# Kernel optimization log

Measured on AMD Instinct MI355X. Metric: run time of the kernel, lower is better.

The kernel has to match this reference:

```python
import jax, jax.numpy as jnp
import numpy as np

HIDDEN = 512
HEADS = 8
HEAD_SIZE = HIDDEN // HEADS
INF = 10000.0


def _heads(x):
    # [N, L, D] -> [N, L, H, Dh]
    return x.reshape(x.shape[0], x.shape[1], HEADS, HEAD_SIZE)


def _alpha_from_logits(logits, mask_row, mask_col):
    # logits: [N, L1, L2, H]; mask_row: [N, L1]; mask_col: [N, L2]
    pair = (mask_row[:, :, None, None] * mask_col[:, None, :, None]) > 0  # [N,L1,L2,1]
    logits = jnp.where(pair, logits, logits - INF)
    alpha = jax.nn.softmax(logits, axis=2)
    row = (mask_row[:, :, None, None]) > 0  # [N,L1,1,1]
    return jnp.where(row, alpha, jnp.zeros_like(alpha))


def setup_inputs() -> dict:
    key = jax.random.key(0)
    ks = jax.random.split(key, 10)
    N, L1, L2, D = 4, 1024, 1024, HIDDEN
    input1 = jax.random.normal(ks[0], (N, L1, D), dtype=jnp.float32)
    input2 = jax.random.normal(ks[1], (N, L2, D), dtype=jnp.float32)
    # masks: 1 for valid tokens, with some padding at the tail
    mask1 = (jnp.arange(L1)[None, :] < jnp.array([L1, L1 - 64, L1 - 128, L1 - 200])[:, None]).astype(jnp.float32)
    mask2 = (jnp.arange(L2)[None, :] < jnp.array([L2 - 32, L2, L2 - 96, L2 - 10])[:, None]).astype(jnp.float32)
    s = 1.0 / np.sqrt(D)
    Wq1 = jax.random.normal(ks[2], (D, D), dtype=jnp.float32) * s
    Wk1 = jax.random.normal(ks[3], (D, D), dtype=jnp.float32) * s
    Wv1 = jax.random.normal(ks[4], (D, D), dtype=jnp.float32) * s
    Wq2 = jax.random.normal(ks[5], (D, D), dtype=jnp.float32) * s
    Wk2 = jax.random.normal(ks[6], (D, D), dtype=jnp.float32) * s
    Wv2 = jax.random.normal(ks[7], (D, D), dtype=jnp.float32) * s
    return {"input1": input1, "mask1": mask1, "input2": input2, "mask2": mask2,
            "Wq1": Wq1, "Wk1": Wk1, "Wv1": Wv1, "Wq2": Wq2, "Wk2": Wk2, "Wv2": Wv2}


def reference(input1, mask1, input2, mask2, Wq1, Wk1, Wv1, Wq2, Wk2, Wv2):
    # nn.Linear(bias=False): x @ W.T
    q1 = _heads(input1 @ Wq1.T)
    k1 = _heads(input1 @ Wk1.T)
    v1 = _heads(input1 @ Wv1.T)
    q2 = _heads(input2 @ Wq2.T)
    k2 = _heads(input2 @ Wk2.T)
    v2 = _heads(input2 @ Wv2.T)
    logits11 = jnp.einsum('blhd,bkhd->blkh', q1, k1)
    logits12 = jnp.einsum('blhd,bkhd->blkh', q1, k2)
    logits21 = jnp.einsum('blhd,bkhd->blkh', q2, k1)
    logits22 = jnp.einsum('blhd,bkhd->blkh', q2, k2)
    a11 = _alpha_from_logits(logits11, mask1, mask1)
    a12 = _alpha_from_logits(logits12, mask1, mask2)
    a21 = _alpha_from_logits(logits21, mask2, mask1)
    a22 = _alpha_from_logits(logits22, mask2, mask2)
    N, L1 = input1.shape[0], input1.shape[1]
    L2 = input2.shape[1]
    o11 = jnp.einsum('blkh,bkhd->blhd', a11, v1).reshape(N, L1, HIDDEN)
    o12 = jnp.einsum('blkh,bkhd->blhd', a12, v2).reshape(N, L1, HIDDEN)
    o21 = jnp.einsum('blkh,bkhd->blhd', a21, v1).reshape(N, L2, HIDDEN)
    o22 = jnp.einsum('blkh,bkhd->blhd', a22, v2).reshape(N, L2, HIDDEN)
    output1 = (o11 + o12) / 2
    output2 = (o21 + o22) / 2
    return (output1, output2)
```

## Files before the change

kernel.cpp:

```cpp
#include <hip/hip_runtime.h>

#define DEV static __device__ __forceinline__

typedef unsigned short u16;
typedef short bf16x8 __attribute__((ext_vector_type(8)));
typedef u16 u16x8v __attribute__((ext_vector_type(8)));
typedef u16 u16x4v __attribute__((ext_vector_type(4)));
typedef float f32x4 __attribute__((ext_vector_type(4)));

static constexpr int NB = 4, L = 1024, D = 512, H = 8, DH = 64;
static constexpr size_t E  = (size_t)NB * L * D;
static constexpr size_t WE = (size_t)D * D;

static constexpr size_t OFF_X1H = 0;
static constexpr size_t OFF_X1L = OFF_X1H + E;
static constexpr size_t OFF_X2H = OFF_X1L + E;
static constexpr size_t OFF_X2L = OFF_X2H + E;
static constexpr size_t OFF_WH  = OFF_X2L + E;
static constexpr size_t OFF_WL  = OFF_WH + 6 * WE;
static constexpr size_t OFF_QKV = OFF_WL + 6 * WE;
static constexpr size_t OFF_VLEN = OFF_QKV + 10 * E;

DEV u16 f2bf(float x) {
    unsigned u = __builtin_bit_cast(unsigned, x);
    unsigned r = u + 0x7FFFu + ((u >> 16) & 1u);
    return (u16)(r >> 16);
}
DEV float bf2f(u16 h) {
    unsigned u = ((unsigned)h) << 16;
    return __builtin_bit_cast(float, u);
}
DEV unsigned cvtpk(float lo, float hi) {
    unsigned r;
    asm("v_cvt_pk_bf16_f32 %0, %1, %2" : "=v"(r) : "v"(lo), "v"(hi));
    return r;
}
DEV bf16x8 ldfrag(const u16* p) {
    u16x8v t = *reinterpret_cast<const u16x8v*>(p);
    return __builtin_bit_cast(bf16x8, t);
}
typedef __attribute__((address_space(1))) const unsigned gas_u32;
typedef __attribute__((address_space(3))) unsigned las_u32;
DEV void gld16(const u16* g, u16* l) {
    __builtin_amdgcn_global_load_lds((gas_u32*)g, (las_u32*)l, 16, 0, 0);
}

__global__ __launch_bounds__(256) void k_split_all(const float* __restrict__ x1,
                                                   const float* __restrict__ x2,
                                                   const float* w0, const float* w1,
                                                   const float* w2, const float* w3,
                                                   const float* w4, const float* w5,
                                                   u16* __restrict__ ws) {
    int b = blockIdx.x;
    const float* src;
    u16 *hi, *lo;
    int i0;
    if (b < 2048)      { src = x1; hi = ws + OFF_X1H; lo = ws + OFF_X1L; i0 = b; }
    else if (b < 4096) { src = x2; hi = ws + OFF_X2H; lo = ws + OFF_X2L; i0 = b - 2048; }
    else {
        int wi = (b - 4096) >> 8;
        const float* wp[6] = {w0, w1, w2, w3, w4, w5};
        src = wp[wi];
        hi = ws + OFF_WH + (size_t)wi * WE;
        lo = ws + OFF_WL + (size_t)wi * WE;
        i0 = (b - 4096) & 255;
    }
    int i = i0 * 256 + threadIdx.x;
    float4 v = reinterpret_cast<const float4*>(src)[i];
    float xs[4] = {v.x, v.y, v.z, v.w};
    u16x4v h, l;
#pragma unroll
    for (int j = 0; j < 4; j++) {
        u16 hh = f2bf(xs[j]);
        h[j] = hh;
        l[j] = f2bf(xs[j] - bf2f(hh));
    }
    int idx = i * 4;
    int m = idx >> 9, e = idx & 511;
    int o = (m << 9) | (e ^ ((m & 7) << 3));
    *reinterpret_cast<u16x4v*>(hi + o) = h;
    *reinterpret_cast<u16x4v*>(lo + o) = l;
}

__global__ __launch_bounds__(256) void k_vlen(const float* __restrict__ m1,
                                              const float* __restrict__ m2,
                                              int* __restrict__ vl) {
    int b = blockIdx.x;
    int s = b >> 2, n = b & 3;
    const float* m = (s ? m2 : m1) + n * L;
    float p = 0.f;
    for (int i = threadIdx.x; i < L; i += 256) p += m[i];
#pragma unroll
    for (int mk = 1; mk < 64; mk <<= 1) p += __shfl_xor(p, mk, 64);
    __shared__ float w4[4];
    if ((threadIdx.x & 63) == 0) w4[threadIdx.x >> 6] = p;
    __syncthreads();
    if (threadIdx.x == 0) vl[b] = (int)(w4[0] + w4[1] + w4[2] + w4[3] + 0.5f);
}

__global__ __launch_bounds__(256) void k_proj(u16* __restrict__ ws) {
    __shared__ __align__(16) u16 ta[2][128][64];
    __shared__ __align__(16) u16 tb[2][128][64];

    const int b     = blockIdx.x;
    const int proj  = b >> 7;
    const int rem   = b & 127;
    const int mtile = rem >> 2;
    const int ntile = rem & 3;
    const int tid   = threadIdx.x;
    const int w     = tid >> 6;
    const int lane  = tid & 63;
    const int lr    = lane & 15;
    const int g     = lane >> 4;
    const int wr    = w >> 1, wc = w & 1;

    const int src  = proj / 3;
    const int kind = proj % 3;
    const u16* Xh = ws + (src ? OFF_X2H : OFF_X1H);
    const u16* Xl = ws + (src ? OFF_X2L : OFF_X1L);
    const u16* Wh = ws + OFF_WH + (size_t)proj * WE;
    const u16* Wl = ws + OFF_WL + (size_t)proj * WE;

    const int m0 = mtile * 128, n0 = ntile * 128;

    const int lrow = lane >> 3, lcol = lane & 7;
    const u16* gA0 = Xh + (size_t)(m0 + w * 32 + lrow) * 512 + lcol * 8;
    const u16* gA1 = Xl + (size_t)(m0 + w * 32 + lrow) * 512 + lcol * 8;
    const u16* gB0 = Wh + (size_t)(n0 + w * 32 + lrow) * 512 + lcol * 8;
    const u16* gB1 = Wl + (size_t)(n0 + w * 32 + lrow) * 512 + lcol * 8;

    f32x4 acc[4][4];
#pragma unroll
    for (int fr = 0; fr < 4; fr++)
#pragma unroll
        for (int cb = 0; cb < 4; cb++) acc[fr][cb] = {0.f, 0.f, 0.f, 0.f};

#pragma unroll 1
    for (int step = 0; step < 8; step++) {
        __syncthreads();
#pragma unroll
        for (int i = 0; i < 4; i++) {
            const int roff = w * 32 + i * 8;
            const int e0 = step * 64;
            gld16(gA0 + e0 + i * (8 * 512), &ta[0][roff][0]);
            gld16(gA1 + e0 + i * (8 * 512), &ta[1][roff][0]);
            gld16(gB0 + e0 + i * (8 * 512), &tb[0][roff][0]);
            gld16(gB1 + e0 + i * (8 * 512), &tb[1][roff][0]);
        }
        __syncthreads();

#pragma unroll
        for (int ks = 0; ks < 2; ks++) {
            bf16x8 ah[4], al[4];
#pragma unroll
            for (int fr = 0; fr < 4; fr++) {
                const int row = wr * 64 + fr * 16 + lr;
                const int ch = (ks * 4 + g) ^ (row & 7);
                ah[fr] = ldfrag(&ta[0][row][ch * 8]);
                al[fr] = ldfrag(&ta[1][row][ch * 8]);
            }
#pragma unroll
            for (int cb = 0; cb < 4; cb++) {
                const int rowb = wc * 64 + cb * 16 + lr;
                const int chb = (ks * 4 + g) ^ (rowb & 7);
                bf16x8 bh = ldfrag(&tb[0][rowb][chb * 8]);
                bf16x8 bl = ldfrag(&tb[1][rowb][chb * 8]);
#pragma unroll
                for (int fr = 0; fr < 4; fr++) {
                    acc[fr][cb] = __builtin_amdgcn_mfma_f32_16x16x32_bf16(ah[fr], bh, acc[fr][cb], 0, 0, 0);
                    acc[fr][cb] = __builtin_amdgcn_mfma_f32_16x16x32_bf16(ah[fr], bl, acc[fr][cb], 0, 0, 0);
                    acc[fr][cb] = __builtin_amdgcn_mfma_f32_16x16x32_bf16(al[fr], bh, acc[fr][cb], 0, 0, 0);
                }
            }
        }
    }

    if (kind < 2) {
        const float qscale = (kind == 0) ? 1.4426950408889634f : 1.0f;
        u16* dhi = ws + OFF_QKV + (size_t)(src * 4 + kind * 2) * E;
        u16* dlo = dhi + E;
#pragma unroll
        for (int fr = 0; fr < 4; fr++)
#pragma unroll
            for (int cb = 0; cb < 4; cb++) {
                int d  = n0 + wc * 64 + cb * 16 + lr;
                int hh = d >> 6, dh = d & 63;
#pragma unroll
                for (int r = 0; r < 4; r++) {
                    int m = m0 + wr * 64 + fr * 16 + g * 4 + r;
                    int n = m >> 10, li = m & 1023;
                    int dhs = kind ? (dh ^ ((li & 7) << 3)) : dh;
                    size_t idx = ((size_t)(n * H + hh) * L + li) * DH + dhs;
                    float v = acc[fr][cb][r] * qscale;
                    u16 hv = f2bf(v);
                    dhi[idx] = hv;
                    dlo[idx] = f2bf(v - bf2f(hv));
                }
            }
    } else {
        u16* vt = ws + OFF_QKV + (size_t)(8 + src) * E;
#pragma unroll
        for (int fr = 0; fr < 4; fr++)
#pragma unroll
            for (int cb = 0; cb < 4; cb++) {
                int d  = n0 + wc * 64 + cb * 16 + lr;
                int hh = d >> 6, dh = d & 63;
                int m  = m0 + wr * 64 + fr * 16 + g * 4;
                int n  = m >> 10, li = m & 1023;
                int lis = li ^ (((dh >> 2) & 3) << 3);
                u16x4v pk;
#pragma unroll
                for (int r = 0; r < 4; r++) pk[r] = f2bf(acc[fr][cb][r]);
                *reinterpret_cast<u16x4v*>(vt + ((size_t)(n * H + hh) * DH + dh) * L + lis) = pk;
            }
    }
}

__global__ __launch_bounds__(512, 4) void k_attn(const u16* __restrict__ ws,
                                                 float* __restrict__ out) {
    __shared__ __align__(16) u16 kbuf[2][2][2][32][64];
    __shared__ __align__(16) u16 vbuf[2][2][64][32];
    __shared__ __align__(16) u16 plds[8][16][32];

    const int bid  = blockIdx.x;
    const int b    = ((bid & 7) << 7) | (bid >> 3);
    const int oi   = b >> 9;
    const int rem  = b & 511;
    const int qt   = rem & 15;
    const int hh   = (rem >> 4) & 7;
    const int n    = rem >> 7;
    const int tid  = threadIdx.x;
    const int w    = tid >> 6;
    const int s    = w >> 2;
    const int wq   = w & 3;
    const int lane = tid & 63;
    const int lr   = lane & 15;
    const int g    = lane >> 4;
    const int swz  = ((lr >> 1) & 3) << 3;
    const int tsw  = (lr >> 2) & 3;

    const size_t nh = (size_t)(n * H + hh);
    const u16* Qh = ws + OFF_QKV + (size_t)(oi * 4) * E;
    const u16* Ql = Qh + E;
    const int* vl = (const int*)(ws + OFF_VLEN);
    const int vls = vl[s * 4 + n];
    const int vlo = vl[oi * 4 + n];

    const int l0 = qt * 64 + wq * 16;
    const size_t qbase = (nh * L + l0 + lr) * DH + g * 8;
    bf16x8 qh0 = ldfrag(Qh + qbase), qh1 = ldfrag(Qh + qbase + 32);
    bf16x8 ql0 = ldfrag(Ql + qbase), ql1 = ldfrag(Ql + qbase + 32);

    float lrun = 0.f;
    f32x4 oacc[4];
#pragma unroll
    for (int d = 0; d < 4; d++) oacc[d] = {0.f, 0.f, 0.f, 0.f};

    const int nkt0 = (vl[n] + 31) >> 5;
    const int nkt1 = (vl[4 + n] + 31) >> 5;
    const int mykt = s ? nkt1 : nkt0;
    const int nktmax = nkt0 > nkt1 ? nkt0 : nkt1;

    const u16* gsrc[3];
    u16* ldst[3];
    int ginc[3], lstr[3];
#pragma unroll
    for (int i = 0; i < 3; i++) {
        const int c  = w * 3 + i;
        const int cs = c / 12, cr = c % 12;
        if (cr < 8) {
            const int hl = cr >> 2, rr = cr & 3;
            const u16* K = ws + OFF_QKV + (size_t)(2 + cs * 4 + hl) * E;
            gsrc[i] = K + (nh * L + rr * 8 + (lane >> 3)) * DH + (lane & 7) * 8;
            ldst[i] = &kbuf[0][cs][hl][rr * 8][0];
            ginc[i] = 32 * DH;
            lstr[i] = 2 * 2 * 32 * 64;
        } else {
            const int rr = cr - 8;
            const u16* V = ws + OFF_QKV + (size_t)(8 + cs) * E;
            gsrc[i] = V + (nh * DH + rr * 16 + (lane >> 2)) * L + (lane & 3) * 8;
            ldst[i] = &vbuf[0][cs][rr * 16][0];
            ginc[i] = 32;
            lstr[i] = 2 * 64 * 32;
        }
    }

#pragma unroll
    for (int i = 0; i < 3; i++) { gld16(gsrc[i], ldst[i]); gsrc[i] += ginc[i]; }
    __syncthreads();

    int cur = 0;
    const int srcb = (lane & 48) + ((lane >> 4) << 2);

#pragma unroll 1
    for (int kt = 0; kt < nktmax; kt++) {
        if (kt + 1 < nktmax) {
            const int nb = cur ^ 1;
#pragma unroll
            for (int i = 0; i < 3; i++) { gld16(gsrc[i], ldst[i] + nb * lstr[i]); gsrc[i] += ginc[i]; }
        }

        if (kt < mykt) {
            __builtin_amdgcn_s_setprio(1);
            f32x4 sfr[2];
#pragma unroll
            for (int j = 0; j < 2; j++) {
                const int row = j * 16 + lr;
                const int t0 = g ^ (row & 7);
                const int t1 = (g + 4) ^ (row & 7);
                bf16x8 kh0 = ldfrag(&kbuf[cur][s][0][row][t0 * 8]);
                bf16x8 kh1 = ldfrag(&kbuf[cur][s][0][row][t1 * 8]);
                bf16x8 kl0 = ldfrag(&kbuf[cur][s][1][row][t0 * 8]);
                bf16x8 kl1 = ldfrag(&kbuf[cur][s][1][row][t1 * 8]);
                f32x4 a = {0.f, 0.f, 0.f, 0.f};
                a = __builtin_amdgcn_mfma_f32_16x16x32_bf16(kh0, qh0, a, 0, 0, 0);
                a = __builtin_amdgcn_mfma_f32_16x16x32_bf16(kh1, qh1, a, 0, 0, 0);
                a = __builtin_amdgcn_mfma_f32_16x16x32_bf16(kl0, qh0, a, 0, 0, 0);
                a = __builtin_amdgcn_mfma_f32_16x16x32_bf16(kl1, qh1, a, 0, 0, 0);
                a = __builtin_amdgcn_mfma_f32_16x16x32_bf16(kh0, ql0, a, 0, 0, 0);
                a = __builtin_amdgcn_mfma_f32_16x16x32_bf16(kh1, ql1, a, 0, 0, 0);
                sfr[j] = a;
            }
            __builtin_amdgcn_s_setprio(0);
            if ((kt << 5) + 32 > vls) {
                const int kb0 = (kt << 5) + g * 4;
#pragma unroll
                for (int j = 0; j < 2; j++)
#pragma unroll
                    for (int r = 0; r < 4; r++)
                        if (kb0 + j * 16 + r >= vls) sfr[j][r] = -1e30f;
            }
            float ps = 0.f;
#pragma unroll
            for (int j = 0; j < 2; j++) {
                float e0 = __builtin_amdgcn_exp2f(sfr[j][0]);
                float e1 = __builtin_amdgcn_exp2f(sfr[j][1]);
                float e2 = __builtin_amdgcn_exp2f(sfr[j][2]);
                float e3 = __builtin_amdgcn_exp2f(sfr[j][3]);
                ps += (e0 + e1) + (e2 + e3);
                uint2 pk;
                pk.x = cvtpk(e0, e1);
                pk.y = cvtpk(e2, e3);
                *reinterpret_cast<uint2*>(&plds[w][lr][(j * 16 + g * 4) ^ swz]) = pk;
            }
            lrun += ps;
            const int base = (g * 8) ^ swz;
            u16x8v pt = *reinterpret_cast<const u16x8v*>(&plds[w][lr][base]);
            bf16x8 pa = __builtin_bit_cast(bf16x8, pt);
            const int t = g ^ tsw;
            __builtin_amdgcn_s_setprio(1);
#pragma unroll
            for (int d = 0; d < 4; d++) {
                const int dh = d * 16 + lr;
                bf16x8 v8 = ldfrag(&vbuf[cur][s][dh][t * 8]);
                oacc[d] = __builtin_amdgcn_mfma_f32_16x16x32_bf16(pa, v8, oacc[d], 0, 0, 0);
            }
            __builtin_amdgcn_s_setprio(0);
        }
        __syncthreads();
        cur ^= 1;
    }

    lrun += __shfl_xor(lrun, 16, 64);
    lrun += __shfl_xor(lrun, 32, 64);
    float lq[4];
#pragma unroll
    for (int r = 0; r < 4; r++) lq[r] = __shfl(lrun, srcb + r, 64);
    float ofin[4][4];
#pragma unroll
    for (int r = 0; r < 4; r++) {
        float inv = __builtin_amdgcn_rcpf(lq[r]);
#pragma unroll
        for (int d = 0; d < 4; d++) ofin[d][r] = oacc[d][r] * inv;
    }

    float (*comb)[16][64] = (float(*)[16][64])&kbuf[0][0][0][0][0];
    if (s == 0) {
#pragma unroll
        for (int d = 0; d < 4; d++)
#pragma unroll
            for (int r = 0; r < 4; r++) comb[wq][g * 4 + r][d * 16 + lr] = ofin[d][r];
    }
    __syncthreads();
    if (s == 1) {
        float* ob = out + (size_t)oi * ((size_t)NB * L * D);
#pragma unroll
        for (int r = 0; r < 4; r++) {
            int row = l0 + g * 4 + r;
#pragma unroll
            for (int d = 0; d < 4; d++) {
                float v = 0.5f * (ofin[d][r] + comb[wq][g * 4 + r][d * 16 + lr]);
                v = (row < vlo) ? v : 0.f;
                ob[((size_t)n * L + row) * D + hh * DH + d * 16 + lr] = v;
            }
        }
    }
}

extern "C" void kernel_launch(void* const* d_in, const int* in_sizes, int n_in,
                              void* d_out, int out_size, void* d_ws, size_t ws_size,
                              hipStream_t stream) {
    const float* input1 = (const float*)d_in[0];
    const float* mask1  = (const float*)d_in[1];
    const float* input2 = (const float*)d_in[2];
    const float* mask2  = (const float*)d_in[3];
    u16*   ws  = (u16*)d_ws;
    float* out = (float*)d_out;

    k_split_all<<<5632, 256, 0, stream>>>(input1, input2,
                                          (const float*)d_in[4], (const float*)d_in[5],
                                          (const float*)d_in[6], (const float*)d_in[7],
                                          (const float*)d_in[8], (const float*)d_in[9], ws);
    k_vlen<<<8, 256, 0, stream>>>(mask1, mask2, (int*)(ws + OFF_VLEN));
    k_proj<<<768, 256, 0, stream>>>(ws);
    k_attn<<<1024, 512, 0, stream>>>(ws, out);
}
```

Baseline: 133.6 us.

## Single-buffer K tile and split barriers to halve LDS and raise occupancy

The K shared-memory buffer drops from double to single buffering. The per-iteration sync is split into two barriers: one after waiting for global loads, before QK^T, and one after the K fragments are read, after which the next K tile is prefetched. V stays double-buffered and its prefetch is issued at the top of the loop. The smaller LDS footprint allows launch bounds of 8 blocks per CU instead of 4, trading an extra barrier and a less hidden K load latency for higher occupancy.

Result: slower. 461.2 us (+245.1%).

```diff
diff --git a/kernel.cpp b/kernel.cpp
--- a/kernel.cpp
+++ b/kernel.cpp
@@ -216,9 +216,9 @@
     }
 }
 
-__global__ __launch_bounds__(512, 4) void k_attn(const u16* __restrict__ ws,
+__global__ __launch_bounds__(512, 8) void k_attn(const u16* __restrict__ ws,
                                                  float* __restrict__ out) {
-    __shared__ __align__(16) u16 kbuf[2][2][2][32][64];
+    __shared__ __align__(16) u16 kbuf[2][2][32][64];
     __shared__ __align__(16) u16 vbuf[2][2][64][32];
     __shared__ __align__(16) u16 plds[8][16][32];
 
@@ -261,57 +261,54 @@
     const int mykt = s ? nkt1 : nkt0;
     const int nktmax = nkt0 > nkt1 ? nkt0 : nkt1;
 
-    const u16* gsrc[3];
-    u16* ldst[3];
-    int ginc[3], lstr[3];
-#pragma unroll
-    for (int i = 0; i < 3; i++) {
-        const int c  = w * 3 + i;
-        const int cs = c / 12, cr = c % 12;
-        if (cr < 8) {
-            const int hl = cr >> 2, rr = cr & 3;
-            const u16* K = ws + OFF_QKV + (size_t)(2 + cs * 4 + hl) * E;
-            gsrc[i] = K + (nh * L + rr * 8 + (lane >> 3)) * DH + (lane & 7) * 8;
-            ldst[i] = &kbuf[0][cs][hl][rr * 8][0];
-            ginc[i] = 32 * DH;
-            lstr[i] = 2 * 2 * 32 * 64;
-        } else {
-            const int rr = cr - 8;
-            const u16* V = ws + OFF_QKV + (size_t)(8 + cs) * E;
-            gsrc[i] = V + (nh * DH + rr * 16 + (lane >> 2)) * L + (lane & 3) * 8;
-            ldst[i] = &vbuf[0][cs][rr * 16][0];
-            ginc[i] = 32;
-            lstr[i] = 2 * 64 * 32;
-        }
-    }
-
-#pragma unroll
-    for (int i = 0; i < 3; i++) { gld16(gsrc[i], ldst[i]); gsrc[i] += ginc[i]; }
-    __syncthreads();
+    const u16 *gK0, *gK1, *gV;
+    u16 *ldK0, *ldK1, *ldV;
+    {
+        const int ck0 = w * 2, ck1 = w * 2 + 1;
+        const int cs0 = ck0 >> 3, hl0 = (ck0 >> 2) & 1, rr0 = ck0 & 3;
+        const int cs1 = ck1 >> 3, hl1 = (ck1 >> 2) & 1, rr1 = ck1 & 3;
+        const u16* K0 = ws + OFF_QKV + (size_t)(2 + cs0 * 4 + hl0) * E;
+        const u16* K1 = ws + OFF_QKV + (size_t)(2 + cs1 * 4 + hl1) * E;
+        gK0 = K0 + (nh * L + rr0 * 8 + (lane >> 3)) * DH + (lane & 7) * 8;
+        gK1 = K1 + (nh * L + rr1 * 8 + (lane >> 3)) * DH + (lane & 7) * 8;
+        ldK0 = &kbuf[cs0][hl0][rr0 * 8][0];
+        ldK1 = &kbuf[cs1][hl1][rr1 * 8][0];
+        const int vcs = w >> 2, vrr = w & 3;
+        const u16* V = ws + OFF_QKV + (size_t)(8 + vcs) * E;
+        gV  = V + (nh * DH + vrr * 16 + (lane >> 2)) * L + (lane & 3) * 8;
+        ldV = &vbuf[0][vcs][vrr * 16][0];
+    }
+    constexpr int VSTR = 2 * 64 * 32;
+    constexpr int KINC = 32 * DH;
+
+    gld16(gV, ldV); gV += 32;
+    gld16(gK0, ldK0); gK0 += KINC;
+    gld16(gK1, ldK1); gK1 += KINC;
 
     int cur = 0;
     const int srcb = (lane & 48) + ((lane >> 4) << 2);
 
 #pragma unroll 1
     for (int kt = 0; kt < nktmax; kt++) {
-        if (kt + 1 < nktmax) {
-            const int nb = cur ^ 1;
-#pragma unroll
-            for (int i = 0; i < 3; i++) { gld16(gsrc[i], ldst[i] + nb * lstr[i]); gsrc[i] += ginc[i]; }
-        }
-
-        if (kt < mykt) {
+        const bool more = kt + 1 < nktmax;
+        asm volatile("s_waitcnt vmcnt(0)" ::: "memory");
+        __builtin_amdgcn_s_barrier();
+        __builtin_amdgcn_sched_barrier(0);
+        if (more) { gld16(gV, ldV + (cur ^ 1) * VSTR); gV += 32; }
+
+        const bool active = kt < mykt;
+        f32x4 sfr[2];
+        if (active) {
             __builtin_amdgcn_s_setprio(1);
-            f32x4 sfr[2];
 #pragma unroll
             for (int j = 0; j < 2; j++) {
                 const int row = j * 16 + lr;
                 const int t0 = g ^ (row & 7);
                 const int t1 = (g + 4) ^ (row & 7);
-                bf16x8 kh0 = ldfrag(&kbuf[cur][s][0][row][t0 * 8]);
-                bf16x8 kh1 = ldfrag(&kbuf[cur][s][0][row][t1 * 8]);
-                bf16x8 kl0 = ldfrag(&kbuf[cur][s][1][row][t0 * 8]);
-                bf16x8 kl1 = ldfrag(&kbuf[cur][s][1][row][t1 * 8]);
+                bf16x8 kh0 = ldfrag(&kbuf[s][0][row][t0 * 8]);
+                bf16x8 kh1 = ldfrag(&kbuf[s][0][row][t1 * 8]);
+                bf16x8 kl0 = ldfrag(&kbuf[s][1][row][t0 * 8]);
+                bf16x8 kl1 = ldfrag(&kbuf[s][1][row][t1 * 8]);
                 f32x4 a = {0.f, 0.f, 0.f, 0.f};
                 a = __builtin_amdgcn_mfma_f32_16x16x32_bf16(kh0, qh0, a, 0, 0, 0);
                 a = __builtin_amdgcn_mfma_f32_16x16x32_bf16(kh1, qh1, a, 0, 0, 0);
@@ -322,6 +319,16 @@
                 sfr[j] = a;
             }
             __builtin_amdgcn_s_setprio(0);
+        }
+        asm volatile("s_waitcnt lgkmcnt(0)" ::: "memory");
+        __builtin_amdgcn_s_barrier();
+        __builtin_amdgcn_sched_barrier(0);
+        if (more) {
+            gld16(gK0, ldK0); gK0 += KINC;
+            gld16(gK1, ldK1); gK1 += KINC;
+        }
+
+        if (active) {
             if ((kt << 5) + 32 > vls) {
                 const int kb0 = (kt << 5) + g * 4;
 #pragma unroll
@@ -357,7 +364,6 @@
             }
             __builtin_amdgcn_s_setprio(0);
         }
-        __syncthreads();
         cur ^= 1;
     }
 
@@ -374,7 +380,8 @@
         for (int d = 0; d < 4; d++) ofin[d][r] = oacc[d][r] * inv;
     }
 
-    float (*comb)[16][64] = (float(*)[16][64])&kbuf[0][0][0][0][0];
+    __syncthreads();
+    float (*comb)[16][64] = (float(*)[16][64])&kbuf[0][0][0][0];
     if (s == 0) {
 #pragma unroll
         for (int d = 0; d < 4; d++)
```
